# Performance work log

Measured on AMD Instinct MI355X. Metric: run time of the kernel, lower is better.

The kernel has to match this reference:

```python
import jax, jax.numpy as jnp
import numpy as np

I, H, NH, A = 128, 2048, 2, 4   # input_size, hidden_size, n_hidden, alpha_dim
K = 2 * A * A                   # per-position theta entries
B = 8192


def make_masks():
    # MADE sequential-ordering masks, identical to DART.create_masks
    inp = np.arange(I)
    degrees = [inp] + [np.arange(H) % (I - 1) for _ in range(NH + 1)] + [np.arange(I) - 1]
    masks = [(d1[:, None] >= d0[None, :]).astype(np.float32)
             for d0, d1 in zip(degrees[:-1], degrees[1:])]
    # last mask repeated per theta entry: repeat(1, K).view(-1, H) == row-repeat
    masks[-1] = np.repeat(masks[-1], K, axis=0)
    return [jnp.asarray(m) for m in masks]


def setup_inputs() -> dict:
    key = jax.random.key(0)
    ks = jax.random.split(key, 5)
    x = jax.random.normal(ks[0], (B, I), dtype=jnp.float32)

    def lin(k, out_dim, in_dim):
        kw, kb = jax.random.split(k)
        s = 1.0 / np.sqrt(in_dim)
        W = jax.random.uniform(kw, (out_dim, in_dim), minval=-s, maxval=s, dtype=jnp.float32)
        b = jax.random.uniform(kb, (out_dim,), minval=-s, maxval=s, dtype=jnp.float32)
        return W, b

    W0, b0 = lin(ks[1], H, I)
    W1, b1 = lin(ks[2], H, H)
    W2, b2 = lin(ks[3], H, H)
    W3, b3 = lin(ks[4], I * K, H)
    return dict(x=x, W0=W0, b0=b0, W1=W1, b1=b1, W2=W2, b2=b2, W3=W3, b3=b3)


def logexpmm(a, b):
    # log-domain matmul: out[..., i, j] = logsumexp_k(a[..., i, k] + b[..., k, j])
    return jax.nn.logsumexp(a[..., :, :, None] + b[..., None, :, :], axis=-2)


def reference(x, W0, b0, W1, b1, W2, b2, W3, b3):
    m = make_masks()
    h = jax.nn.relu(x @ (m[0] * W0).T + b0)
    h = jax.nn.relu(h @ (m[1] * W1).T + b1)
    h = jax.nn.relu(h @ (m[2] * W2).T + b2)
    theta = (h @ (m[3] * W3).T + b3).reshape(-1, I, 2, A, A)
    mu, alpha = theta[:, :, 0], theta[:, :, 1]  # (B, I, A, A)

    LOG2PI = float(np.log(2.0 * np.pi))
    xe = x[:, :, None, None]
    # Normal(mu, exp(alpha)).log_prob(x) - log(alpha_dim)
    logp = (-0.5 * ((xe - mu) * jnp.exp(-alpha)) ** 2
            - alpha - 0.5 * LOG2PI - jnp.log(jnp.float32(A)))

    first = logp[:, 0, 0:1]        # (B, 1, A)
    last = logp[:, -1, :, 0:1]     # (B, A, 1)
    inner = jnp.swapaxes(logp[:, 1:-1], 0, 1)  # (I-2, B, A, A)

    def step(carry, mtx):
        return logexpmm(carry, mtx), None

    prod, _ = jax.lax.scan(step, inner[0], inner[1:])
    return logexpmm(first, logexpmm(prod, last))  # (B, 1, 1)
```

## Files before the change

kernel.cpp:

```cpp
#include <hip/hip_runtime.h>
#include <hip/hip_bf16.h>
#include <cstdint>
#include <cstddef>

#define AS1 __attribute__((address_space(1)))
#define AS3 __attribute__((address_space(3)))

typedef __bf16 bf16x8 __attribute__((ext_vector_type(8)));
typedef float  floatx4 __attribute__((ext_vector_type(4)));

__device__ __forceinline__ void load_lds16(const void* g, void* l) {
    __builtin_amdgcn_global_load_lds((AS1 void*)g, (AS3 void*)l, 16, 0, 0);
}

__device__ __forceinline__ float fexp2(float x) { return __builtin_amdgcn_exp2f(x); }
__device__ __forceinline__ float flog2(float x) { return __builtin_amdgcn_logf(x); }

__device__ __forceinline__ int invp(int p) {
    return p < 2032 ? (p & 15) * 127 + (p >> 4) : p;
}
__device__ __forceinline__ int resp(int p) {
    return p < 2032 ? (p >> 4) : p - 2032;
}

__global__ __launch_bounds__(256)
void prep_all(const float* __restrict__ x,  const float* __restrict__ W0,
              const float* __restrict__ W1, const float* __restrict__ W2,
              const float* __restrict__ W3,
              __bf16* __restrict__ xb,  __bf16* __restrict__ w0m,
              __bf16* __restrict__ w1m, __bf16* __restrict__ w2m,
              __bf16* __restrict__ w3m)
{
    __shared__ float lds[2048];
    const int blk = blockIdx.x;
    const int tid = threadIdx.x;
    const int t8  = tid * 8;

    if (blk < 640) {
        bf16x8 o;
        if (blk < 512) {
            size_t base = (size_t)blk * 2048 + t8;
            floatx4 a = *(const floatx4*)(x + base);
            floatx4 b = *(const floatx4*)(x + base + 4);
#pragma unroll
            for (int j = 0; j < 4; ++j) { o[j] = (__bf16)a[j]; o[4 + j] = (__bf16)b[j]; }
            *(bf16x8*)(xb + base) = o;
        } else {
            long idx = (long)(blk - 512) * 2048 + t8;
            int p_n = (int)(idx >> 7);
            int c   = (int)(idx & 127);
            int dg  = resp(p_n);
            const float* s = W0 + (long)invp(p_n) * 128 + c;
            floatx4 a = *(const floatx4*)s;
            floatx4 b = *(const floatx4*)(s + 4);
#pragma unroll
            for (int j = 0; j < 8; ++j) {
                float v = j < 4 ? a[j] : b[j - 4];
                o[j] = (__bf16)((dg >= c + j) ? v : 0.0f);
            }
            *(bf16x8*)(w0m + idx) = o;
        }
        return;
    }

    const float* srow; __bf16* drow; int deg_n; bool strict;
    if (blk < 2688) {
        int p_n = blk - 640;
        srow = W1 + (size_t)invp(p_n) * 2048; drow = w1m + (size_t)p_n * 2048;
        deg_n = resp(p_n); strict = false;
    } else if (blk < 4736) {
        int p_n = blk - 2688;
        srow = W2 + (size_t)invp(p_n) * 2048; drow = w2m + (size_t)p_n * 2048;
        deg_n = resp(p_n); strict = false;
    } else {
        int n = blk - 4736;
        srow = W3 + (size_t)n * 2048; drow = w3m + (size_t)n * 2048;
        deg_n = n >> 5; strict = true;
    }
    floatx4 a = *(const floatx4*)(srow + t8);
    floatx4 b = *(const floatx4*)(srow + t8 + 4);
    *(floatx4*)&lds[t8]     = a;
    *(floatx4*)&lds[t8 + 4] = b;
    __syncthreads();
    bf16x8 o;
#pragma unroll
    for (int j = 0; j < 8; ++j) {
        int p = t8 + j;
        float v = lds[invp(p)];
        int dg = resp(p);
        bool keep = strict ? (deg_n > dg) : (deg_n >= dg);
        o[j] = (__bf16)(keep ? v : 0.0f);
    }
    *(bf16x8*)(drow + t8) = o;
}

template <bool RELU, bool OBF16, bool TLAYOUT, bool PERMBIAS>
__global__ __launch_bounds__(256, 3)
void gemm_bt(const __bf16* __restrict__ A, const __bf16* __restrict__ Bw,
             const float* __restrict__ bias, void* __restrict__ Cout,
             int N, int K, int klm, int kla, int kls, int tail)
{
    __shared__ __align__(16) __bf16 lsA[128 * 64];
    __shared__ __align__(16) __bf16 lsB[128 * 64];
    const int tid  = threadIdx.x;
    const int wave = tid >> 6;
    const int lane = tid & 63;
    const int bm = blockIdx.x;
    const int bn = (gridDim.y - 1) - blockIdx.y;
    const int wm = wave >> 1, wn = wave & 1;

    const int r8 = lane >> 3;
    const int cb = (lane & 7) ^ r8;
    const __bf16* gsrc[8];
    __bf16* ldst[8];
#pragma unroll
    for (int t = 0; t < 8; ++t) {
        int j = wave * 8 + t;
        if (j < 16) {
            int row = bm * 128 + j * 8 + r8;
            gsrc[t] = A + (size_t)row * K + cb * 8;
            ldst[t] = lsA + j * 512;
        } else {
            int jj = j - 16;
            int row = bn * 128 + jj * 8 + r8;
            gsrc[t] = Bw + (size_t)row * K + cb * 8;
            ldst[t] = lsB + jj * 512;
        }
    }

    const int fr  = lane & 15;
    const int ks  = lane >> 4;
    const int sx  = fr & 7;
    const int sl0 = ((ks)     ^ sx) * 8;
    const int sl1 = ((4 + ks) ^ sx) * 8;
    const __bf16* arow[4];
    const __bf16* brow[4];
#pragma unroll
    for (int i = 0; i < 4; ++i) {
        arow[i] = lsA + (wm * 64 + i * 16 + fr) * 64;
        brow[i] = lsB + (wn * 64 + i * 16 + fr) * 64;
    }

    floatx4 acc[4][4];
    const floatx4 vzero = {0.f, 0.f, 0.f, 0.f};
#pragma unroll
    for (int mi = 0; mi < 4; ++mi)
#pragma unroll
        for (int ni = 0; ni < 4; ++ni) acc[mi][ni] = vzero;

    const int nk = K >> 6;
    int limit = (klm * bn + kla) >> kls;
    if (limit > nk) limit = nk;
    const int iters = limit + ((tail && limit < nk) ? 1 : 0);

    for (int it = 0; it < iters; ++it) {
        const int kt = (it < limit ? it : nk - 1) << 6;
        __syncthreads();
#pragma unroll
        for (int t = 0; t < 8; ++t)
            load_lds16((const void*)(gsrc[t] + kt), (void*)ldst[t]);
        __syncthreads();
        bf16x8 af[4], bf[4];
#pragma unroll
        for (int i = 0; i < 4; ++i) af[i] = *(const bf16x8*)(arow[i] + sl0);
#pragma unroll
        for (int i = 0; i < 4; ++i) bf[i] = *(const bf16x8*)(brow[i] + sl0);
#pragma unroll
        for (int mi = 0; mi < 4; ++mi)
#pragma unroll
            for (int ni = 0; ni < 4; ++ni)
                acc[mi][ni] = __builtin_amdgcn_mfma_f32_16x16x32_bf16(
                    af[mi], bf[ni], acc[mi][ni], 0, 0, 0);
#pragma unroll
        for (int i = 0; i < 4; ++i) af[i] = *(const bf16x8*)(arow[i] + sl1);
#pragma unroll
        for (int i = 0; i < 4; ++i) bf[i] = *(const bf16x8*)(brow[i] + sl1);
#pragma unroll
        for (int mi = 0; mi < 4; ++mi)
#pragma unroll
            for (int ni = 0; ni < 4; ++ni)
                acc[mi][ni] = __builtin_amdgcn_mfma_f32_16x16x32_bf16(
                    af[mi], bf[ni], acc[mi][ni], 0, 0, 0);
    }

    const int cn  = lane & 15;
    const int cr4 = (lane >> 4) * 4;
#pragma unroll
    for (int ni = 0; ni < 4; ++ni) {
        int col = bn * 128 + wn * 64 + ni * 16 + cn;
        float bv = bias[PERMBIAS ? invp(col) : col];
#pragma unroll
        for (int mi = 0; mi < 4; ++mi) {
            int row0 = bm * 128 + wm * 64 + mi * 16 + cr4;
#pragma unroll
            for (int q = 0; q < 4; ++q) {
                float v = acc[mi][ni][q] + bv;
                if (RELU) v = fmaxf(v, 0.f);
                if (TLAYOUT) {
                    size_t addr = (size_t)(bm * 2 + wm) * ((size_t)N * 64)
                                + (size_t)col * 64 + (mi * 16 + cr4 + q);
                    ((__bf16*)Cout)[addr] = (__bf16)v;
                } else if (OBF16) {
                    ((__bf16*)Cout)[(size_t)(row0 + q) * N + col] = (__bf16)v;
                } else {
                    ((float*)Cout)[(size_t)(row0 + q) * N + col] = v;
                }
            }
        }
    }
}

__global__ __launch_bounds__(256)
void chain_seg(const __bf16* __restrict__ th2,
               const float* __restrict__ x,
               float* __restrict__ P)
{
    const int b = blockIdx.x * 256 + threadIdx.x;
    const int s = blockIdx.y;
    const int i0 = 1 + s * 7;
    const __bf16* tp = th2 + (size_t)(b >> 6) * (4096 * 64) + (b & 63)
                           + (size_t)i0 * 32 * 64;
    const float* xp = x + (size_t)b * 128 + i0;

    const float LOG2E = 1.4426950408889634f;
    const float C0    = 2.3052328943245633f;

    float M[4][4];
#pragma unroll
    for (int r = 0; r < 4; ++r)
#pragma unroll
        for (int c = 0; c < 4; ++c) M[r][c] = (r == c) ? 0.f : -1e30f;

    for (int ii = 0; ii < 7; ++ii) {
        float mu[16], al[16];
#pragma unroll
        for (int j = 0; j < 16; ++j) mu[j] = (float)tp[(size_t)j * 64];
#pragma unroll
        for (int j = 0; j < 16; ++j) al[j] = (float)tp[(size_t)(16 + j) * 64];
        float xv = xp[ii];
        tp += 32 * 64;
        float lp[16];
#pragma unroll
        for (int j = 0; j < 16; ++j) {
            float a = al[j];
            float e = fexp2(-a * LOG2E);
            float z = (xv - mu[j]) * e;
            lp[j] = (-0.5f * z * z - a - C0) * LOG2E;
        }
        float Mn[4][4];
#pragma unroll
        for (int r = 0; r < 4; ++r)
#pragma unroll
            for (int c = 0; c < 4; ++c) {
                float a0 = M[r][0] + lp[0 * 4 + c];
                float a1 = M[r][1] + lp[1 * 4 + c];
                float a2 = M[r][2] + lp[2 * 4 + c];
                float a3 = M[r][3] + lp[3 * 4 + c];
                float mx = fmaxf(fmaxf(a0, a1), fmaxf(a2, a3));
                float sm = fexp2(a0 - mx) + fexp2(a1 - mx) +
                           fexp2(a2 - mx) + fexp2(a3 - mx);
                Mn[r][c] = mx + flog2(sm);
            }
#pragma unroll
        for (int r = 0; r < 4; ++r)
#pragma unroll
            for (int c = 0; c < 4; ++c) M[r][c] = Mn[r][c];
    }

    float* pb = P + ((size_t)b * 18 + s) * 16;
#pragma unroll
    for (int r = 0; r < 4; ++r) {
        floatx4 o = {M[r][0], M[r][1], M[r][2], M[r][3]};
        *(floatx4*)(pb + r * 4) = o;
    }
}

__global__ __launch_bounds__(256)
void chain_fin(const __bf16* __restrict__ th2,
               const float* __restrict__ x,
               const float* __restrict__ P,
               float* __restrict__ out)
{
    const int tid  = threadIdx.x;
    const int lane = tid & 63;
    const int r    = lane & 3;
    const int l0   = lane & 60;
    const int b    = blockIdx.x * 64 + (tid >> 2);
    const __bf16* tb = th2 + (size_t)(b >> 6) * (4096 * 64) + (b & 63);

    const float LOG2E = 1.4426950408889634f;
    const float LN2   = 0.6931471805599453f;
    const float C0    = 2.3052328943245633f;

    const float* Pb = P + (size_t)b * 288;
    floatx4 m0 = *(const floatx4*)(Pb + r * 4);
    float M[4] = {m0[0], m0[1], m0[2], m0[3]};

#pragma unroll
    for (int s = 1; s < 18; ++s) {
        floatx4 lr = *(const floatx4*)(Pb + s * 16 + r * 4);
        float Mn[4];
#pragma unroll
        for (int c = 0; c < 4; ++c) {
            float a0 = M[0] + __shfl(lr[c], l0 + 0);
            float a1 = M[1] + __shfl(lr[c], l0 + 1);
            float a2 = M[2] + __shfl(lr[c], l0 + 2);
            float a3 = M[3] + __shfl(lr[c], l0 + 3);
            float mx = fmaxf(fmaxf(a0, a1), fmaxf(a2, a3));
            float sm = fexp2(a0 - mx) + fexp2(a1 - mx) + fexp2(a2 - mx) + fexp2(a3 - mx);
            Mn[c] = mx + flog2(sm);
        }
#pragma unroll
        for (int k = 0; k < 4; ++k) M[k] = Mn[k];
    }

    float xl = x[(size_t)b * 128 + 127];
    float a[4];
#pragma unroll
    for (int c = 0; c < 4; ++c) {
        float mu_ = (float)tb[(size_t)(4064 + c * 4) * 64];
        float al_ = (float)tb[(size_t)(4064 + 16 + c * 4) * 64];
        float e = fexp2(-al_ * LOG2E);
        float z = (xl - mu_) * e;
        float lp2 = (-0.5f * z * z - al_ - C0) * LOG2E;
        a[c] = M[c] + lp2;
    }
    float mx = fmaxf(fmaxf(a[0], a[1]), fmaxf(a[2], a[3]));
    float tr = mx + flog2(fexp2(a[0] - mx) + fexp2(a[1] - mx) +
                          fexp2(a[2] - mx) + fexp2(a[3] - mx));

    float x0  = x[(size_t)b * 128];
    float muf = (float)tb[(size_t)r * 64];
    float alf = (float)tb[(size_t)(16 + r) * 64];
    float ef = fexp2(-alf * LOG2E);
    float zf = (x0 - muf) * ef;
    float f2 = (-0.5f * zf * zf - alf - C0) * LOG2E;
    float v = f2 + tr;
    float m1 = fmaxf(v, __shfl_xor(v, 1));
    float m2 = fmaxf(m1, __shfl_xor(m1, 2));
    float sum = fexp2(v - m2);
    sum += __shfl_xor(sum, 1);
    sum += __shfl_xor(sum, 2);
    if (r == 0) out[b] = (m2 + flog2(sum)) * LN2;
}

extern "C" void kernel_launch(void* const* d_in, const int* in_sizes, int n_in,
                              void* d_out, int out_size, void* d_ws, size_t ws_size,
                              hipStream_t stream)
{
    (void)in_sizes; (void)n_in; (void)out_size; (void)ws_size;
    const float* x  = (const float*)d_in[0];
    const float* W0 = (const float*)d_in[1];
    const float* b0 = (const float*)d_in[2];
    const float* W1 = (const float*)d_in[3];
    const float* b1 = (const float*)d_in[4];
    const float* W2 = (const float*)d_in[5];
    const float* b2 = (const float*)d_in[6];
    const float* W3 = (const float*)d_in[7];
    const float* b3 = (const float*)d_in[8];

    char* ws = (char*)d_ws;
    size_t off = 0;
    auto alloc = [&](size_t bytes) { char* p = ws + off; off += bytes; return p; };
    __bf16* xb  = (__bf16*)alloc((size_t)8192 * 128 * 2);
    __bf16* w0m = (__bf16*)alloc((size_t)2048 * 128 * 2);
    __bf16* w1m = (__bf16*)alloc((size_t)2048 * 2048 * 2);
    __bf16* w2m = (__bf16*)alloc((size_t)2048 * 2048 * 2);
    __bf16* w3m = (__bf16*)alloc((size_t)4096 * 2048 * 2);
    __bf16* h1  = (__bf16*)alloc((size_t)8192 * 2048 * 2);
    __bf16* h2  = (__bf16*)alloc((size_t)8192 * 2048 * 2);
    __bf16* th  = (__bf16*)alloc((size_t)8192 * 4096 * 2);
    __bf16* h3  = h1;
    float*  P   = (float*)h2;

    prep_all<<<8832, 256, 0, stream>>>(x, W0, W1, W2, W3, xb, w0m, w1m, w2m, w3m);

    gemm_bt<true, true, false, true><<<dim3(64, 16), 256, 0, stream>>>(
        xb, w0m, b0, h1, 2048, 128, 8, 71, 6, 0);
    gemm_bt<true, true, false, true><<<dim3(64, 16), 256, 0, stream>>>(
        h1, w1m, b1, h2, 2048, 2048, 2, 2, 0, 1);
    gemm_bt<true, true, false, true><<<dim3(64, 16), 256, 0, stream>>>(
        h2, w2m, b2, h3, 2048, 2048, 2, 2, 0, 1);
    gemm_bt<false, false, true, false><<<dim3(64, 32), 256, 0, stream>>>(
        h3, w3m, b3, th, 4096, 2048, 1, 1, 0, 1);

    chain_seg<<<dim3(32, 18), 256, 0, stream>>>(th, x, P);
    chain_fin<<<128, 256, 0, stream>>>(th, x, P, (float*)d_out);
}
```

Measured before the change: 323.8 us.

## Sort hidden units by MADE degree to drop tail tile and tighten K limits

Replaces the hidden-unit permutation with one that fully sorts all 2048 units by degree, including the 16 leftover units previously placed at the end. Each GEMM can then compute its exact K-tile bound from cumulative degree counts, with no extra tail iteration covering the last K tile. This cuts wasted MFMA work on the masked triangular weights. Launch bounds also rise to 4 blocks per CU, which may increase register pressure and spilling.

Result: no change. 326.5 us (+0.8%).

```diff
diff --git a/kernel.cpp b/kernel.cpp
--- a/kernel.cpp
+++ b/kernel.cpp
@@ -16,11 +16,17 @@
 __device__ __forceinline__ float fexp2(float x) { return __builtin_amdgcn_exp2f(x); }
 __device__ __forceinline__ float flog2(float x) { return __builtin_amdgcn_logf(x); }
 
-__device__ __forceinline__ int invp(int p) {
-    return p < 2032 ? (p & 15) * 127 + (p >> 4) : p;
-}
-__device__ __forceinline__ int resp(int p) {
-    return p < 2032 ? (p >> 4) : p - 2032;
+__device__ __forceinline__ int resp_s(int p) {
+    return p < 272 ? p / 17 : 16 + ((p - 272) >> 4);
+}
+__device__ __forceinline__ int invp_s(int p) {
+    if (p < 272) { int d = p / 17; int r = p - d * 17;
+                   return r < 16 ? d + r * 127 : 2032 + d; }
+    int d = 16 + ((p - 272) >> 4); int j = (p - 272) & 15;
+    return d + j * 127;
+}
+__device__ __forceinline__ int cnt_le(int D) {
+    return D < 16 ? (D + 1) * 17 : 272 + ((D - 15) << 4);
 }
 
 __global__ __launch_bounds__(256)
@@ -49,8 +55,8 @@
             long idx = (long)(blk - 512) * 2048 + t8;
             int p_n = (int)(idx >> 7);
             int c   = (int)(idx & 127);
-            int dg  = resp(p_n);
-            const float* s = W0 + (long)invp(p_n) * 128 + c;
+            int dg  = resp_s(p_n);
+            const float* s = W0 + (long)invp_s(p_n) * 128 + c;
             floatx4 a = *(const floatx4*)s;
             floatx4 b = *(const floatx4*)(s + 4);
 #pragma unroll
@@ -66,12 +72,12 @@
     const float* srow; __bf16* drow; int deg_n; bool strict;
     if (blk < 2688) {
         int p_n = blk - 640;
-        srow = W1 + (size_t)invp(p_n) * 2048; drow = w1m + (size_t)p_n * 2048;
-        deg_n = resp(p_n); strict = false;
+        srow = W1 + (size_t)invp_s(p_n) * 2048; drow = w1m + (size_t)p_n * 2048;
+        deg_n = resp_s(p_n); strict = false;
     } else if (blk < 4736) {
         int p_n = blk - 2688;
-        srow = W2 + (size_t)invp(p_n) * 2048; drow = w2m + (size_t)p_n * 2048;
-        deg_n = resp(p_n); strict = false;
+        srow = W2 + (size_t)invp_s(p_n) * 2048; drow = w2m + (size_t)p_n * 2048;
+        deg_n = resp_s(p_n); strict = false;
     } else {
         int n = blk - 4736;
         srow = W3 + (size_t)n * 2048; drow = w3m + (size_t)n * 2048;
@@ -86,19 +92,19 @@
 #pragma unroll
     for (int j = 0; j < 8; ++j) {
         int p = t8 + j;
-        float v = lds[invp(p)];
-        int dg = resp(p);
+        float v = lds[invp_s(p)];
+        int dg = resp_s(p);
         bool keep = strict ? (deg_n > dg) : (deg_n >= dg);
         o[j] = (__bf16)(keep ? v : 0.0f);
     }
     *(bf16x8*)(drow + t8) = o;
 }
 
-template <bool RELU, bool OBF16, bool TLAYOUT, bool PERMBIAS>
-__global__ __launch_bounds__(256, 3)
+template <bool RELU, bool OBF16, bool TLAYOUT, bool PERMBIAS, int LMODE>
+__global__ __launch_bounds__(256, 4)
 void gemm_bt(const __bf16* __restrict__ A, const __bf16* __restrict__ Bw,
              const float* __restrict__ bias, void* __restrict__ Cout,
-             int N, int K, int klm, int kla, int kls, int tail)
+             int N, int K)
 {
     __shared__ __align__(16) __bf16 lsA[128 * 64];
     __shared__ __align__(16) __bf16 lsB[128 * 64];
@@ -149,12 +155,15 @@
         for (int ni = 0; ni < 4; ++ni) acc[mi][ni] = vzero;
 
     const int nk = K >> 6;
-    int limit = (klm * bn + kla) >> kls;
+    int limit;
+    if (LMODE == 0)      limit = (cnt_le(resp_s(bn * 128 + 127)) + 63) >> 6;
+    else if (LMODE == 1) { int D = 4 * bn + 2; if (D > 126) D = 126;
+                           limit = (cnt_le(D) + 63) >> 6; }
+    else                 limit = (resp_s(bn * 128 + 127) + 64) >> 6;
     if (limit > nk) limit = nk;
-    const int iters = limit + ((tail && limit < nk) ? 1 : 0);
-
-    for (int it = 0; it < iters; ++it) {
-        const int kt = (it < limit ? it : nk - 1) << 6;
+
+    for (int it = 0; it < limit; ++it) {
+        const int kt = it << 6;
         __syncthreads();
 #pragma unroll
         for (int t = 0; t < 8; ++t)
@@ -188,7 +197,7 @@
 #pragma unroll
     for (int ni = 0; ni < 4; ++ni) {
         int col = bn * 128 + wn * 64 + ni * 16 + cn;
-        float bv = bias[PERMBIAS ? invp(col) : col];
+        float bv = bias[PERMBIAS ? invp_s(col) : col];
 #pragma unroll
         for (int mi = 0; mi < 4; ++mi) {
             int row0 = bm * 128 + wm * 64 + mi * 16 + cr4;
@@ -375,14 +384,14 @@
 
     prep_all<<<8832, 256, 0, stream>>>(x, W0, W1, W2, W3, xb, w0m, w1m, w2m, w3m);
 
-    gemm_bt<true, true, false, true><<<dim3(64, 16), 256, 0, stream>>>(
-        xb, w0m, b0, h1, 2048, 128, 8, 71, 6, 0);
-    gemm_bt<true, true, false, true><<<dim3(64, 16), 256, 0, stream>>>(
-        h1, w1m, b1, h2, 2048, 2048, 2, 2, 0, 1);
-    gemm_bt<true, true, false, true><<<dim3(64, 16), 256, 0, stream>>>(
-        h2, w2m, b2, h3, 2048, 2048, 2, 2, 0, 1);
-    gemm_bt<false, false, true, false><<<dim3(64, 32), 256, 0, stream>>>(
-        h3, w3m, b3, th, 4096, 2048, 1, 1, 0, 1);
+    gemm_bt<true, true, false, true, 2><<<dim3(64, 16), 256, 0, stream>>>(
+        xb, w0m, b0, h1, 2048, 128);
+    gemm_bt<true, true, false, true, 0><<<dim3(64, 16), 256, 0, stream>>>(
+        h1, w1m, b1, h2, 2048, 2048);
+    gemm_bt<true, true, false, true, 0><<<dim3(64, 16), 256, 0, stream>>>(
+        h2, w2m, b2, h3, 2048, 2048);
+    gemm_bt<false, false, true, false, 1><<<dim3(64, 32), 256, 0, stream>>>(
+        h3, w3m, b3, th, 4096, 2048);
 
     chain_seg<<<dim3(32, 18), 256, 0, stream>>>(th, x, P);
     chain_fin<<<128, 256, 0, stream>>>(th, x, P, (float*)d_out);
```
